# Performance work log

Measured on AMD Instinct MI355X. Metric: run time of the kernel, lower is better.

Reference implementation:

```python
import jax, jax.numpy as jnp
import numpy as np

B, C, CO = 8, 32, 32            # batch, in_channels, out_channels
NIN, NOUT, D1, D2 = 16, 10, 512, 512  # MLP dims: 16 -> 512 -> 512 -> 10 (L=3)
NRC = (NIN + 2 * NOUT + 6) * C  # rc_inp feature dim = 42*C = 1344


def _conv1(x, W, b):
    # 1x1 Conv1d: x (b, Cin, N) -> (b, Cout, N)
    return jnp.einsum('oi,bin->bon', W, x) + b[None, :, None]


def _lin(x, W, b):
    return x @ W.T + b


def setup_inputs() -> dict:
    key = jax.random.key(0)
    ks = iter(jax.random.split(key, 64))
    def rn(shape, s=1.0):
        return jax.random.normal(next(ks), shape, dtype=jnp.float32) * s
    return {
        'w0': rn((B, C, D1, NIN)), 'w1': rn((B, C, D2, D1)), 'w2': rn((B, C, NOUT, D2)),
        'b0': rn((B, C, D1)), 'b1': rn((B, C, D2)), 'b2': rn((B, C, NOUT)),
        'W_w0_rpt': rn((NIN * CO, (NIN + 2) * C), 0.02), 'B_w0_rpt': rn((NIN * CO,), 0.02),
        'W_w0_rc': rn((NIN * CO, NRC), 0.02), 'B_w0_rc': rn((NIN * CO,), 0.02),
        'W_b0': rn((CO, (NIN + 2) * C), 0.02), 'B_b0': rn((CO,), 0.02),
        'W_b0_rc': rn((CO, NRC), 0.02), 'B_b0_rc': rn((CO,), 0.02),
        'W_l1': rn((CO, C), 0.02), 'B_l1': rn((CO,), 0.02),
        'W_l1_rc': rn((CO, NRC), 0.02), 'B_l1_rc': rn((CO,), 0.02),
        'W_l1_r': rn((CO, (3 + NIN) * C), 0.02), 'B_l1_r': rn((CO,), 0.02),
        'W_l1_c': rn((CO, (3 + NOUT) * C), 0.02), 'B_l1_c': rn((CO,), 0.02),
        'W_bias1': rn((CO, (3 + NOUT) * C), 0.02), 'B_bias1': rn((CO,), 0.02),
        'W_bias1_rc': rn((CO, NRC), 0.02), 'B_bias1_rc': rn((CO,), 0.02),
        'W_fin_cpt': rn((NOUT * CO, (NOUT + 1) * C), 0.02), 'B_fin_cpt': rn((NOUT * CO,), 0.02),
        'W_fin_rc': rn((NOUT * CO, NRC), 0.02), 'B_fin_rc': rn((NOUT * CO,), 0.02),
        'W_bfin_rc': rn((NOUT * CO, NRC), 0.02), 'B_bfin_rc': rn((NOUT * CO,), 0.02),
    }


def reference(w0, w1, w2, b0, b1, b2,
              W_w0_rpt, B_w0_rpt, W_w0_rc, B_w0_rc, W_b0, B_b0, W_b0_rc, B_b0_rc,
              W_l1, B_l1, W_l1_rc, B_l1_rc, W_l1_r, B_l1_r, W_l1_c, B_l1_c,
              W_bias1, B_bias1, W_bias1_rc, B_bias1_rc,
              W_fin_cpt, B_fin_cpt, W_fin_rc, B_fin_rc, W_bfin_rc, B_bfin_rc):
    b = w0.shape[0]
    cm0, cm1, cm2 = w0.mean(-1), w1.mean(-1), w2.mean(-1)  # col means (b,c,n_row)
    rm0, rm1, rm2 = w0.mean(-2), w1.mean(-2), w2.mean(-2)  # row means (b,c,n_col)
    rc = jnp.concatenate([
        w0.mean((-1, -2)), w1.mean((-1, -2)), w2.mean((-1, -2)),
        b0.mean(-1), b1.mean(-1), b2.mean(-1),
        rm0.reshape(b, -1), cm2.reshape(b, -1), b2.reshape(b, -1)], axis=-1)  # (b, NRC)
    # ---- layer 0 (row-pointwise + rc broadcast) ----
    rpt = jnp.concatenate([jnp.swapaxes(w0, -1, -2).reshape(b, C * NIN, D1), rm1, b0], axis=1)
    z0 = _conv1(rpt, W_w0_rpt, B_w0_rpt) + _lin(rc, W_w0_rc, B_w0_rc)[..., None]
    zw0 = jnp.swapaxes(z0.reshape(b, CO, NIN, D1), -1, -2)  # (b, co, D1, NIN)
    u0 = _conv1(rpt, W_b0, B_b0) + _lin(rc, W_b0_rc, B_b0_rc)[..., None]  # (b, co, D1)
    # ---- middle layer (pointwise + rc + row + col broadcasts) ----
    row_b = jnp.concatenate([rm1, cm0, b0, jnp.swapaxes(w0, -1, -2).reshape(b, C * NIN, D1)], axis=1)
    col_b = jnp.concatenate([cm1, b1, rm2, w2.reshape(b, C * NOUT, D2)], axis=1)
    zw1 = (jnp.einsum('oi,bihw->bohw', W_l1, w1) + B_l1[None, :, None, None]
           + _lin(rc, W_l1_rc, B_l1_rc)[..., None, None]
           + _conv1(row_b, W_l1_r, B_l1_r)[:, :, None, :]
           + _conv1(col_b, W_l1_c, B_l1_c)[:, :, :, None])  # (b, co, D2, D1)
    u1 = _conv1(col_b, W_bias1, B_bias1) + _lin(rc, W_bias1_rc, B_bias1_rc)[..., None]  # (b, co, D2)
    # ---- final layer (col-pointwise + rc broadcast) ----
    cpt = jnp.concatenate([w2.reshape(b, C * NOUT, D2), cm1], axis=1)
    zf = _conv1(cpt, W_fin_cpt, B_fin_cpt) + _lin(rc, W_fin_rc, B_fin_rc)[..., None]
    zw2 = zf.reshape(b, CO, NOUT, D2)
    u2 = _lin(rc, W_bfin_rc, B_bfin_rc).reshape(b, CO, NOUT)
    return (zw0, zw1, zw2, u0, u1, u2)
```

## Files before the change

### kernel.cpp

```cpp
#include <hip/hip_runtime.h>

#define OUT_ZW1 2097152u
#define OUT_ZW2 69206016u
#define OUT_U0  70516736u
#define OUT_U1  70647808u
#define OUT_U2  70778880u

#define WS_RM1      0u
#define WS_CM1      131072u
#define WS_CM0      262144u
#define WS_RM2      393216u
#define WS_CM2      524288u
#define WS_RC       526848u
#define WS_TW0      537600u
#define WS_TB0      541696u
#define WS_TL1      541952u
#define WS_TBIAS1   542208u
#define WS_TFIN     542464u
#define WS_RTERM    545024u
#define WS_CTERM    676096u
#define WS_W0T      807168u
#define WS_WT_L1    3330304u

static __device__ __forceinline__ float wave_reduce(float v) {
#pragma unroll
  for (int off = 32; off > 0; off >>= 1) v += __shfl_down(v, off);
  return v;
}

__global__ __launch_bounds__(256) void kprep(
    const float* __restrict__ w0, const float* __restrict__ W_l1,
    float* __restrict__ ws) {
  int blk = blockIdx.x, tid = threadIdx.x;
  if (blk < 554) {
    int i = blk * 256 + tid;
    if (i < 131072) ws[WS_RM1 + i] = 0.f;
    else ws[WS_RC + (i - 131072)] = 0.f;
  } else if (blk < 558) {
    int idx = (blk - 554) * 256 + tid;
    int r = idx >> 5, c = idx & 31;
    ws[WS_WT_L1 + c * 32 + r] = W_l1[idx];
  } else {
    int bc = blk - 558;
    int b = bc >> 5, c = bc & 31;
    for (int k = 0; k < 16; ++k)
      for (int d = tid; d < 512; d += 256)
        ws[WS_W0T + ((size_t)(b * 512 + c * 16 + k)) * 512 + d] =
            w0[((size_t)bc * 512 + d) * 16 + k];
  }
}

__global__ __launch_bounds__(256) void kstats2(
    const float* __restrict__ w0, const float* __restrict__ w2,
    const float* __restrict__ b0, const float* __restrict__ b1,
    const float* __restrict__ b2, const float* __restrict__ w1,
    float* __restrict__ cm0, float* __restrict__ rm2, float* __restrict__ cm2,
    float* __restrict__ rm1, float* __restrict__ cm1, float* __restrict__ rc) {
  __shared__ float sred[16];
  __shared__ float stot;
  __shared__ float rpart[512];
  int tid = threadIdx.x, lane = tid & 63;

  if (blockIdx.x < 256) {
    int bc = blockIdx.x;
    int b = bc >> 5, c = bc & 31;
    float* rcb = rc + b * 1344;

    if (tid < 16) sred[tid] = 0.f;
    if (tid == 0) stot = 0.f;
    __syncthreads();
    {
      float rm0p[16];
#pragma unroll
      for (int k = 0; k < 16; ++k) rm0p[k] = 0.f;
      float tot = 0.f;
      for (int d = tid; d < 512; d += 256) {
        const float4* p = (const float4*)(w0 + ((size_t)bc * 512 + d) * 16);
        float s = 0.f;
#pragma unroll
        for (int q = 0; q < 4; ++q) {
          float4 v = p[q];
          s += v.x + v.y + v.z + v.w;
          rm0p[q * 4 + 0] += v.x; rm0p[q * 4 + 1] += v.y;
          rm0p[q * 4 + 2] += v.z; rm0p[q * 4 + 3] += v.w;
        }
        cm0[(size_t)bc * 512 + d] = s * (1.f / 16.f);
        tot += s;
      }
#pragma unroll
      for (int k = 0; k < 16; ++k) {
        float r = wave_reduce(rm0p[k]);
        if (lane == 0) atomicAdd(&sred[k], r);
      }
      float rt = wave_reduce(tot);
      if (lane == 0) atomicAdd(&stot, rt);
    }
    __syncthreads();
    if (tid < 16) rcb[192 + c * 16 + tid] = sred[tid] * (1.f / 512.f);
    if (tid == 0) rcb[c] = stot * (1.f / 8192.f);
    __syncthreads();

    if (tid < 10) sred[tid] = 0.f;
    if (tid == 0) stot = 0.f;
    __syncthreads();
    {
      float cm2p[10];
#pragma unroll
      for (int k = 0; k < 10; ++k) cm2p[k] = 0.f;
      float tot = 0.f;
      for (int d = tid; d < 512; d += 256) {
        float s = 0.f;
#pragma unroll
        for (int k = 0; k < 10; ++k) {
          float v = w2[((size_t)bc * 10 + k) * 512 + d];
          s += v; cm2p[k] += v;
        }
        rm2[(size_t)bc * 512 + d] = s * 0.1f;
        tot += s;
      }
#pragma unroll
      for (int k = 0; k < 10; ++k) {
        float r = wave_reduce(cm2p[k]);
        if (lane == 0) atomicAdd(&sred[k], r);
      }
      float rt = wave_reduce(tot);
      if (lane == 0) atomicAdd(&stot, rt);
    }
    __syncthreads();
    if (tid < 10) {
      float m = sred[tid] * (1.f / 512.f);
      cm2[bc * 10 + tid] = m;
      rcb[704 + c * 10 + tid] = m;
    }
    if (tid == 0) rcb[64 + c] = stot * (1.f / 5120.f);
    __syncthreads();

    if (tid < 2) sred[tid] = 0.f;
    __syncthreads();
    {
      float t0 = 0.f, t1 = 0.f;
      for (int d = tid; d < 512; d += 256) {
        t0 += b0[(size_t)bc * 512 + d];
        t1 += b1[(size_t)bc * 512 + d];
      }
      t0 = wave_reduce(t0); t1 = wave_reduce(t1);
      if (lane == 0) { atomicAdd(&sred[0], t0); atomicAdd(&sred[1], t1); }
    }
    __syncthreads();
    if (tid == 0) {
      rcb[96 + c] = sred[0] * (1.f / 512.f);
      rcb[128 + c] = sred[1] * (1.f / 512.f);
    }

    float vb2 = 0.f;
    if (tid < 10) {
      vb2 = b2[bc * 10 + tid];
      rcb[1024 + c * 10 + tid] = vb2;
    }
    if (tid < 64) {
      float s = wave_reduce(vb2);
      if (tid == 0) rcb[160 + c] = s * 0.1f;
    }
  } else {
    int idx = blockIdx.x - 256;
    int bc = idx >> 2, hc = idx & 3;
    int b = bc >> 5, c = bc & 31;
    int wid = tid >> 6;
    const float* base = w1 + (size_t)bc * 262144 + (size_t)hc * 128 * 512;
    float col0 = 0.f, col1 = 0.f;
    for (int hl = 0; hl < 128; ++hl) {
      float2 x = *(const float2*)(base + hl * 512 + 2 * tid);
      col0 += x.x; col1 += x.y;
      float r = wave_reduce(x.x + x.y);
      if (lane == 0) rpart[hl * 4 + wid] = r;
    }
    __syncthreads();
    if (tid < 128) {
      float s = rpart[tid * 4] + rpart[tid * 4 + 1] + rpart[tid * 4 + 2] + rpart[tid * 4 + 3];
      cm1[(size_t)bc * 512 + hc * 128 + tid] = s * (1.f / 512.f);
    }
    atomicAdd(&rm1[(size_t)bc * 512 + 2 * tid], col0);
    atomicAdd(&rm1[(size_t)bc * 512 + 2 * tid + 1], col1);
    float bt = wave_reduce(col0 + col1);
    if (lane == 0) atomicAdd(&rc[b * 1344 + 32 + c], bt * (1.f / 262144.f));
  }
}

__global__ __launch_bounds__(256) void krcgemm(
    const float* __restrict__ rc,
    const float* __restrict__ W_w0_rc, const float* __restrict__ B_w0_rc,
    const float* __restrict__ W_b0_rc, const float* __restrict__ B_b0_rc,
    const float* __restrict__ W_l1_rc, const float* __restrict__ B_l1_rc,
    const float* __restrict__ W_bias1_rc, const float* __restrict__ B_bias1_rc,
    const float* __restrict__ W_fin_rc, const float* __restrict__ B_fin_rc,
    const float* __restrict__ W_bfin_rc, const float* __restrict__ B_bfin_rc,
    float* __restrict__ t_w0, float* __restrict__ t_b0, float* __restrict__ t_l1,
    float* __restrict__ t_bias1, float* __restrict__ t_fin, float* __restrict__ u2out) {
  int blk = blockIdx.x;
  int b = blk / 312;
  int tid = threadIdx.x, lane = tid & 63, wid = tid >> 6;
  int r = (blk % 312) * 4 + wid;
  __shared__ float rcs[1344];
  for (int i = tid; i < 1344; i += 256) rcs[i] = rc[b * 1344 + i];
  __syncthreads();
  const float* W; const float* Bb; float* dst; int row;
  if (r < 512)      { W = W_w0_rc;    Bb = B_w0_rc;    row = r;       dst = t_w0 + b * 512; }
  else if (r < 544) { W = W_b0_rc;    Bb = B_b0_rc;    row = r - 512; dst = t_b0 + b * 32; }
  else if (r < 576) { W = W_l1_rc;    Bb = B_l1_rc;    row = r - 544; dst = t_l1 + b * 32; }
  else if (r < 608) { W = W_bias1_rc; Bb = B_bias1_rc; row = r - 576; dst = t_bias1 + b * 32; }
  else if (r < 928) { W = W_fin_rc;   Bb = B_fin_rc;   row = r - 608; dst = t_fin + b * 320; }
  else              { W = W_bfin_rc;  Bb = B_bfin_rc;  row = r - 928; dst = u2out + b * 320; }
  const float* wr = W + (size_t)row * 1344;
  float acc = 0.f;
  for (int j = lane; j < 1344; j += 64) acc += wr[j] * rcs[j];
  acc = wave_reduce(acc);
  if (lane == 0) dst[row] = acc + Bb[row];
}

__global__ __launch_bounds__(256) void kbig(
    const float* __restrict__ rm1, const float* __restrict__ cm0,
    const float* __restrict__ b0, const float* __restrict__ w0T,
    const float* __restrict__ W_l1_r, const float* __restrict__ B_l1_r,
    float* __restrict__ rterm,
    const float* __restrict__ cm1, const float* __restrict__ b1,
    const float* __restrict__ rm2, const float* __restrict__ w2,
    const float* __restrict__ W_l1_c, const float* __restrict__ B_l1_c,
    const float* __restrict__ B_l1, const float* __restrict__ t_l1,
    const float* __restrict__ W_bias1, const float* __restrict__ B_bias1,
    const float* __restrict__ t_bias1,
    float* __restrict__ cterm_full, float* __restrict__ u1out,
    const float* __restrict__ W_w0_rpt, const float* __restrict__ B_rpt,
    const float* __restrict__ W_b0, const float* __restrict__ B_b0w,
    const float* __restrict__ t_w0, const float* __restrict__ t_b0,
    const float* __restrict__ W_fin_cpt, const float* __restrict__ B_fin,
    const float* __restrict__ t_fin, float* __restrict__ out) {
  __shared__ float wlds[6656];
  int bid = blockIdx.x, tid = threadIdx.x;

  if (bid < 128) {
    int x = bid & 1, oy = (bid >> 1) & 7, b = bid >> 4;
    int p = x * 256 + tid;
    if (oy < 4) {
      int o0 = oy * 8;
      for (int idx = tid; idx < 608 * 8; idx += 256) {
        int i = idx >> 3, oo = idx & 7;
        wlds[idx] = W_l1_r[(size_t)(o0 + oo) * 608 + i];
      }
      __syncthreads();
      float acc[8] = {0, 0, 0, 0, 0, 0, 0, 0};
#pragma unroll 4
      for (int i = 0; i < 32; ++i) {
        float xv = rm1[((size_t)b * 32 + i) * 512 + p] * (1.f / 512.f);
        float4 wa = *(const float4*)&wlds[i * 8];
        float4 wb = *(const float4*)&wlds[i * 8 + 4];
        acc[0] += wa.x * xv; acc[1] += wa.y * xv; acc[2] += wa.z * xv; acc[3] += wa.w * xv;
        acc[4] += wb.x * xv; acc[5] += wb.y * xv; acc[6] += wb.z * xv; acc[7] += wb.w * xv;
      }
#pragma unroll 4
      for (int i = 0; i < 32; ++i) {
        float xv = cm0[((size_t)b * 32 + i) * 512 + p];
        float4 wa = *(const float4*)&wlds[(32 + i) * 8];
        float4 wb = *(const float4*)&wlds[(32 + i) * 8 + 4];
        acc[0] += wa.x * xv; acc[1] += wa.y * xv; acc[2] += wa.z * xv; acc[3] += wa.w * xv;
        acc[4] += wb.x * xv; acc[5] += wb.y * xv; acc[6] += wb.z * xv; acc[7] += wb.w * xv;
      }
#pragma unroll 4
      for (int i = 0; i < 32; ++i) {
        float xv = b0[((size_t)b * 32 + i) * 512 + p];
        float4 wa = *(const float4*)&wlds[(64 + i) * 8];
        float4 wb = *(const float4*)&wlds[(64 + i) * 8 + 4];
        acc[0] += wa.x * xv; acc[1] += wa.y * xv; acc[2] += wa.z * xv; acc[3] += wa.w * xv;
        acc[4] += wb.x * xv; acc[5] += wb.y * xv; acc[6] += wb.z * xv; acc[7] += wb.w * xv;
      }
      const float* xp = w0T + (size_t)b * 512 * 512 + p;
#pragma unroll 4
      for (int i = 0; i < 512; ++i) {
        float xv = xp[(size_t)i * 512];
        float4 wa = *(const float4*)&wlds[(96 + i) * 8];
        float4 wb = *(const float4*)&wlds[(96 + i) * 8 + 4];
        acc[0] += wa.x * xv; acc[1] += wa.y * xv; acc[2] += wa.z * xv; acc[3] += wa.w * xv;
        acc[4] += wb.x * xv; acc[5] += wb.y * xv; acc[6] += wb.z * xv; acc[7] += wb.w * xv;
      }
#pragma unroll
      for (int oo = 0; oo < 8; ++oo) {
        int o = o0 + oo;
        rterm[((size_t)b * 32 + o) * 512 + p] = acc[oo] + B_l1_r[o];
      }
    } else {
      int o0 = (oy - 4) * 8;
      for (int idx = tid; idx < 416 * 8; idx += 256) {
        int i = idx >> 3, oo = idx & 7;
        wlds[idx] = W_l1_c[(size_t)(o0 + oo) * 416 + i];
        wlds[3328 + idx] = W_bias1[(size_t)(o0 + oo) * 416 + i];
      }
      __syncthreads();
      float ac[8] = {0, 0, 0, 0, 0, 0, 0, 0};
      float au[8] = {0, 0, 0, 0, 0, 0, 0, 0};
#pragma unroll 4
      for (int i = 0; i < 32; ++i) {
        float xv = cm1[((size_t)b * 32 + i) * 512 + p];
        float4 wa = *(const float4*)&wlds[i * 8];
        float4 wb = *(const float4*)&wlds[i * 8 + 4];
        float4 va = *(const float4*)&wlds[3328 + i * 8];
        float4 vb = *(const float4*)&wlds[3328 + i * 8 + 4];
        ac[0] += wa.x * xv; ac[1] += wa.y * xv; ac[2] += wa.z * xv; ac[3] += wa.w * xv;
        ac[4] += wb.x * xv; ac[5] += wb.y * xv; ac[6] += wb.z * xv; ac[7] += wb.w * xv;
        au[0] += va.x * xv; au[1] += va.y * xv; au[2] += va.z * xv; au[3] += va.w * xv;
        au[4] += vb.x * xv; au[5] += vb.y * xv; au[6] += vb.z * xv; au[7] += vb.w * xv;
      }
#pragma unroll 4
      for (int i = 0; i < 32; ++i) {
        float xv = b1[((size_t)b * 32 + i) * 512 + p];
        float4 wa = *(const float4*)&wlds[(32 + i) * 8];
        float4 wb = *(const float4*)&wlds[(32 + i) * 8 + 4];
        float4 va = *(const float4*)&wlds[3328 + (32 + i) * 8];
        float4 vb = *(const float4*)&wlds[3328 + (32 + i) * 8 + 4];
        ac[0] += wa.x * xv; ac[1] += wa.y * xv; ac[2] += wa.z * xv; ac[3] += wa.w * xv;
        ac[4] += wb.x * xv; ac[5] += wb.y * xv; ac[6] += wb.z * xv; ac[7] += wb.w * xv;
        au[0] += va.x * xv; au[1] += va.y * xv; au[2] += va.z * xv; au[3] += va.w * xv;
        au[4] += vb.x * xv; au[5] += vb.y * xv; au[6] += vb.z * xv; au[7] += vb.w * xv;
      }
#pragma unroll 4
      for (int i = 0; i < 32; ++i) {
        float xv = rm2[((size_t)b * 32 + i) * 512 + p];
        float4 wa = *(const float4*)&wlds[(64 + i) * 8];
        float4 wb = *(const float4*)&wlds[(64 + i) * 8 + 4];
        float4 va = *(const float4*)&wlds[3328 + (64 + i) * 8];
        float4 vb = *(const float4*)&wlds[3328 + (64 + i) * 8 + 4];
        ac[0] += wa.x * xv; ac[1] += wa.y * xv; ac[2] += wa.z * xv; ac[3] += wa.w * xv;
        ac[4] += wb.x * xv; ac[5] += wb.y * xv; ac[6] += wb.z * xv; ac[7] += wb.w * xv;
        au[0] += va.x * xv; au[1] += va.y * xv; au[2] += va.z * xv; au[3] += va.w * xv;
        au[4] += vb.x * xv; au[5] += vb.y * xv; au[6] += vb.z * xv; au[7] += vb.w * xv;
      }
      const float* xp = w2 + (size_t)b * 320 * 512 + p;
#pragma unroll 4
      for (int i = 0; i < 320; ++i) {
        float xv = xp[(size_t)i * 512];
        float4 wa = *(const float4*)&wlds[(96 + i) * 8];
        float4 wb = *(const float4*)&wlds[(96 + i) * 8 + 4];
        float4 va = *(const float4*)&wlds[3328 + (96 + i) * 8];
        float4 vb = *(const float4*)&wlds[3328 + (96 + i) * 8 + 4];
        ac[0] += wa.x * xv; ac[1] += wa.y * xv; ac[2] += wa.z * xv; ac[3] += wa.w * xv;
        ac[4] += wb.x * xv; ac[5] += wb.y * xv; ac[6] += wb.z * xv; ac[7] += wb.w * xv;
        au[0] += va.x * xv; au[1] += va.y * xv; au[2] += va.z * xv; au[3] += va.w * xv;
        au[4] += vb.x * xv; au[5] += vb.y * xv; au[6] += vb.z * xv; au[7] += vb.w * xv;
      }
#pragma unroll
      for (int oo = 0; oo < 8; ++oo) {
        int o = o0 + oo;
        cterm_full[((size_t)b * 32 + o) * 512 + p] = ac[oo] + B_l1_c[o] + B_l1[o] + t_l1[b * 32 + o];
        u1out[((size_t)b * 32 + o) * 512 + p] = au[oo] + B_bias1[o] + t_bias1[b * 32 + o];
      }
    }
  } else if (bid < 1216) {
    int t = bid - 128;
    int x = t & 1, rest = t >> 1;
    int oc = rest % 68, b = rest / 68;
    bool isZ = oc < 64;
    int o0 = isZ ? oc * 8 : (oc - 64) * 8;
    const float* Wsrc = isZ ? W_w0_rpt : W_b0;
    for (int idx = tid; idx < 576 * 8; idx += 256) {
      int i = idx >> 3, oo = idx & 7;
      wlds[idx] = Wsrc[(size_t)(o0 + oo) * 576 + i];
    }
    __syncthreads();
    int d = x * 256 + tid;
    float acc[8] = {0, 0, 0, 0, 0, 0, 0, 0};
    const float* xp = w0T + (size_t)b * 512 * 512 + d;
#pragma unroll 4
    for (int i = 0; i < 512; ++i) {
      float xv = xp[(size_t)i * 512];
      float4 wa = *(const float4*)&wlds[i * 8];
      float4 wb = *(const float4*)&wlds[i * 8 + 4];
      acc[0] += wa.x * xv; acc[1] += wa.y * xv; acc[2] += wa.z * xv; acc[3] += wa.w * xv;
      acc[4] += wb.x * xv; acc[5] += wb.y * xv; acc[6] += wb.z * xv; acc[7] += wb.w * xv;
    }
#pragma unroll 4
    for (int i = 0; i < 32; ++i) {
      float xv = rm1[((size_t)b * 32 + i) * 512 + d] * (1.f / 512.f);
      float4 wa = *(const float4*)&wlds[(512 + i) * 8];
      float4 wb = *(const float4*)&wlds[(512 + i) * 8 + 4];
      acc[0] += wa.x * xv; acc[1] += wa.y * xv; acc[2] += wa.z * xv; acc[3] += wa.w * xv;
      acc[4] += wb.x * xv; acc[5] += wb.y * xv; acc[6] += wb.z * xv; acc[7] += wb.w * xv;
    }
#pragma unroll 4
    for (int i = 0; i < 32; ++i) {
      float xv = b0[((size_t)b * 32 + i) * 512 + d];
      float4 wa = *(const float4*)&wlds[(544 + i) * 8];
      float4 wb = *(const float4*)&wlds[(544 + i) * 8 + 4];
      acc[0] += wa.x * xv; acc[1] += wa.y * xv; acc[2] += wa.z * xv; acc[3] += wa.w * xv;
      acc[4] += wb.x * xv; acc[5] += wb.y * xv; acc[6] += wb.z * xv; acc[7] += wb.w * xv;
    }
    if (isZ) {
#pragma unroll
      for (int oo = 0; oo < 8; ++oo) {
        int o = o0 + oo, co = o >> 4, k = o & 15;
        out[(((size_t)b * 32 + co) * 512 + d) * 16 + k] = acc[oo] + B_rpt[o] + t_w0[b * 512 + o];
      }
    } else {
#pragma unroll
      for (int oo = 0; oo < 8; ++oo) {
        int o = o0 + oo;
        out[OUT_U0 + ((size_t)b * 32 + o) * 512 + d] = acc[oo] + B_b0w[o] + t_b0[b * 32 + o];
      }
    }
  } else {
    int t = bid - 1216;
    int x = t & 1, rest = t >> 1;
    int oc = rest % 40, b = rest / 40;
    int o0 = oc * 8;
    for (int idx = tid; idx < 352 * 8; idx += 256) {
      int i = idx >> 3, oo = idx & 7;
      wlds[idx] = W_fin_cpt[(size_t)(o0 + oo) * 352 + i];
    }
    __syncthreads();
    int d = x * 256 + tid;
    float acc[8] = {0, 0, 0, 0, 0, 0, 0, 0};
    const float* xp = w2 + (size_t)b * 320 * 512 + d;
#pragma unroll 4
    for (int i = 0; i < 320; ++i) {
      float xv = xp[(size_t)i * 512];
      float4 wa = *(const float4*)&wlds[i * 8];
      float4 wb = *(const float4*)&wlds[i * 8 + 4];
      acc[0] += wa.x * xv; acc[1] += wa.y * xv; acc[2] += wa.z * xv; acc[3] += wa.w * xv;
      acc[4] += wb.x * xv; acc[5] += wb.y * xv; acc[6] += wb.z * xv; acc[7] += wb.w * xv;
    }
#pragma unroll 4
    for (int i = 0; i < 32; ++i) {
      float xv = cm1[((size_t)b * 32 + i) * 512 + d];
      float4 wa = *(const float4*)&wlds[(320 + i) * 8];
      float4 wb = *(const float4*)&wlds[(320 + i) * 8 + 4];
      acc[0] += wa.x * xv; acc[1] += wa.y * xv; acc[2] += wa.z * xv; acc[3] += wa.w * xv;
      acc[4] += wb.x * xv; acc[5] += wb.y * xv; acc[6] += wb.z * xv; acc[7] += wb.w * xv;
    }
#pragma unroll
    for (int oo = 0; oo < 8; ++oo) {
      int o = o0 + oo;
      out[OUT_ZW2 + ((size_t)b * 320 + o) * 512 + d] = acc[oo] + B_fin[o] + t_fin[b * 320 + o];
    }
  }
}

__global__ __launch_bounds__(256) void kzw1(
    const float* __restrict__ w1, const float* __restrict__ Wt_l1,
    const float* __restrict__ rterm, const float* __restrict__ cterm,
    float* __restrict__ out) {
  __shared__ float wl[1024];
  int hp = blockIdx.x, b = blockIdx.y;
  int t = threadIdx.x;
  for (int i = t; i < 1024; i += 256) wl[i] = Wt_l1[i];
  __syncthreads();
  int h0 = hp * 2;
  int hoff = t >> 7;
  int w = (t & 127) * 4;
  float4 acc[32];
#pragma unroll
  for (int o = 0; o < 32; ++o) acc[o] = make_float4(0.f, 0.f, 0.f, 0.f);
  const float* src = w1 + ((size_t)b * 32 * 512 + h0) * 512 + 4 * t;
#pragma unroll 4
  for (int i = 0; i < 32; ++i) {
    float4 x = *(const float4*)(src + (size_t)i * 262144);
    const float* wp = wl + i * 32;
#pragma unroll
    for (int o = 0; o < 32; ++o) {
      acc[o].x += wp[o] * x.x;
      acc[o].y += wp[o] * x.y;
      acc[o].z += wp[o] * x.z;
      acc[o].w += wp[o] * x.w;
    }
  }
  int h = h0 + hoff;
#pragma unroll
  for (int o = 0; o < 32; ++o) {
    float cf = cterm[((size_t)b * 32 + o) * 512 + h];
    float4 rt = *(const float4*)(rterm + ((size_t)b * 32 + o) * 512 + w);
    float4 res = make_float4(acc[o].x + rt.x + cf, acc[o].y + rt.y + cf,
                             acc[o].z + rt.z + cf, acc[o].w + rt.w + cf);
    *(float4*)(out + (size_t)OUT_ZW1 + (((size_t)b * 32 + o) * 512 + h) * 512 + w) = res;
  }
}

extern "C" void kernel_launch(void* const* d_in, const int* in_sizes, int n_in,
                              void* d_out, int out_size, void* d_ws, size_t ws_size,
                              hipStream_t stream) {
  const float* w0 = (const float*)d_in[0];
  const float* w1 = (const float*)d_in[1];
  const float* w2 = (const float*)d_in[2];
  const float* b0 = (const float*)d_in[3];
  const float* b1 = (const float*)d_in[4];
  const float* b2 = (const float*)d_in[5];
  const float* W_w0_rpt = (const float*)d_in[6];
  const float* B_w0_rpt = (const float*)d_in[7];
  const float* W_w0_rc = (const float*)d_in[8];
  const float* B_w0_rc = (const float*)d_in[9];
  const float* W_b0 = (const float*)d_in[10];
  const float* B_b0 = (const float*)d_in[11];
  const float* W_b0_rc = (const float*)d_in[12];
  const float* B_b0_rc = (const float*)d_in[13];
  const float* W_l1 = (const float*)d_in[14];
  const float* B_l1 = (const float*)d_in[15];
  const float* W_l1_rc = (const float*)d_in[16];
  const float* B_l1_rc = (const float*)d_in[17];
  const float* W_l1_r = (const float*)d_in[18];
  const float* B_l1_r = (const float*)d_in[19];
  const float* W_l1_c = (const float*)d_in[20];
  const float* B_l1_c = (const float*)d_in[21];
  const float* W_bias1 = (const float*)d_in[22];
  const float* B_bias1 = (const float*)d_in[23];
  const float* W_bias1_rc = (const float*)d_in[24];
  const float* B_bias1_rc = (const float*)d_in[25];
  const float* W_fin_cpt = (const float*)d_in[26];
  const float* B_fin_cpt = (const float*)d_in[27];
  const float* W_fin_rc = (const float*)d_in[28];
  const float* B_fin_rc = (const float*)d_in[29];
  const float* W_bfin_rc = (const float*)d_in[30];
  const float* B_bfin_rc = (const float*)d_in[31];
  float* ws = (float*)d_ws;
  float* out = (float*)d_out;

  kprep<<<dim3(814), 256, 0, stream>>>(w0, W_l1, ws);

  kstats2<<<dim3(1280), 256, 0, stream>>>(w0, w2, b0, b1, b2, w1, ws + WS_CM0,
                                          ws + WS_RM2, ws + WS_CM2, ws + WS_RM1,
                                          ws + WS_CM1, ws + WS_RC);

  krcgemm<<<dim3(8 * 312), 256, 0, stream>>>(
      ws + WS_RC, W_w0_rc, B_w0_rc, W_b0_rc, B_b0_rc, W_l1_rc, B_l1_rc, W_bias1_rc,
      B_bias1_rc, W_fin_rc, B_fin_rc, W_bfin_rc, B_bfin_rc, ws + WS_TW0, ws + WS_TB0,
      ws + WS_TL1, ws + WS_TBIAS1, ws + WS_TFIN, out + OUT_U2);

  kbig<<<dim3(1856), 256, 0, stream>>>(
      ws + WS_RM1, ws + WS_CM0, b0, ws + WS_W0T, W_l1_r, B_l1_r, ws + WS_RTERM,
      ws + WS_CM1, b1, ws + WS_RM2, w2, W_l1_c, B_l1_c, B_l1, ws + WS_TL1, W_bias1,
      B_bias1, ws + WS_TBIAS1, ws + WS_CTERM, out + OUT_U1,
      W_w0_rpt, B_w0_rpt, W_b0, B_b0, ws + WS_TW0, ws + WS_TB0,
      W_fin_cpt, B_fin_cpt, ws + WS_TFIN, out);

  kzw1<<<dim3(256, 8), 256, 0, stream>>>(w1, ws + WS_WT_L1, ws + WS_RTERM, ws + WS_CTERM,
                                         out);
  (void)in_sizes; (void)n_in; (void)out_size; (void)ws_size;
}
```

Before: 364.6 us.

## Fuse prep, stats and rc-GEMM kernels to cut launches and atomics

Five launches become three. The zeroing and transpose kernel is folded into the stats kernel, w0 is transposed with vectorised reads, and the W_l1 transpose is done on load inside kzw1. Atomic accumulation of rm1 and the w1 total is replaced by per-quarter partial buffers that consumers sum, which removes the zero-init pass. The separate rc GEMV kernel is removed: each kbig block computes the rc projections it needs on the fly, and extra blocks produce u2. The cost is redundant rc dot products across blocks and four reads for every rm1 value.

New measurement: 427.2 us. 17.1% more time.

```diff
diff --git a/kernel.cpp b/kernel.cpp
--- a/kernel.cpp
+++ b/kernel.cpp
@@ -6,21 +6,15 @@
 #define OUT_U1  70647808u
 #define OUT_U2  70778880u
 
-#define WS_RM1      0u
-#define WS_CM1      131072u
-#define WS_CM0      262144u
-#define WS_RM2      393216u
-#define WS_CM2      524288u
-#define WS_RC       526848u
-#define WS_TW0      537600u
-#define WS_TB0      541696u
-#define WS_TL1      541952u
-#define WS_TBIAS1   542208u
-#define WS_TFIN     542464u
-#define WS_RTERM    545024u
-#define WS_CTERM    676096u
-#define WS_W0T      807168u
-#define WS_WT_L1    3330304u
+#define WS_RM1P  0u
+#define WS_CM1   524288u
+#define WS_CM0   655360u
+#define WS_RM2   786432u
+#define WS_RCW1  917504u
+#define WS_RC    918528u
+#define WS_RTERM 929280u
+#define WS_CTERM 1060352u
+#define WS_W0T   1191424u
 
 static __device__ __forceinline__ float wave_reduce(float v) {
 #pragma unroll
@@ -28,43 +22,24 @@
   return v;
 }
 
-__global__ __launch_bounds__(256) void kprep(
-    const float* __restrict__ w0, const float* __restrict__ W_l1,
-    float* __restrict__ ws) {
-  int blk = blockIdx.x, tid = threadIdx.x;
-  if (blk < 554) {
-    int i = blk * 256 + tid;
-    if (i < 131072) ws[WS_RM1 + i] = 0.f;
-    else ws[WS_RC + (i - 131072)] = 0.f;
-  } else if (blk < 558) {
-    int idx = (blk - 554) * 256 + tid;
-    int r = idx >> 5, c = idx & 31;
-    ws[WS_WT_L1 + c * 32 + r] = W_l1[idx];
-  } else {
-    int bc = blk - 558;
-    int b = bc >> 5, c = bc & 31;
-    for (int k = 0; k < 16; ++k)
-      for (int d = tid; d < 512; d += 256)
-        ws[WS_W0T + ((size_t)(b * 512 + c * 16 + k)) * 512 + d] =
-            w0[((size_t)bc * 512 + d) * 16 + k];
-  }
-}
-
-__global__ __launch_bounds__(256) void kstats2(
+__global__ __launch_bounds__(256) void ksetup(
     const float* __restrict__ w0, const float* __restrict__ w2,
     const float* __restrict__ b0, const float* __restrict__ b1,
     const float* __restrict__ b2, const float* __restrict__ w1,
-    float* __restrict__ cm0, float* __restrict__ rm2, float* __restrict__ cm2,
-    float* __restrict__ rm1, float* __restrict__ cm1, float* __restrict__ rc) {
+    float* __restrict__ ws) {
   __shared__ float sred[16];
   __shared__ float stot;
   __shared__ float rpart[512];
+  __shared__ float swsum[4];
   int tid = threadIdx.x, lane = tid & 63;
-
-  if (blockIdx.x < 256) {
-    int bc = blockIdx.x;
+  int bx = blockIdx.x;
+
+  if (bx < 256) {
+    int bc = bx;
     int b = bc >> 5, c = bc & 31;
-    float* rcb = rc + b * 1344;
+    float* rcb = ws + WS_RC + b * 1344;
+    float* cm0 = ws + WS_CM0;
+    float* rm2 = ws + WS_RM2;
 
     if (tid < 16) sred[tid] = 0.f;
     if (tid == 0) stot = 0.f;
@@ -127,11 +102,7 @@
       if (lane == 0) atomicAdd(&stot, rt);
     }
     __syncthreads();
-    if (tid < 10) {
-      float m = sred[tid] * (1.f / 512.f);
-      cm2[bc * 10 + tid] = m;
-      rcb[704 + c * 10 + tid] = m;
-    }
+    if (tid < 10) rcb[704 + c * 10 + tid] = sred[tid] * (1.f / 512.f);
     if (tid == 0) rcb[64 + c] = stot * (1.f / 5120.f);
     __syncthreads();
 
@@ -161,12 +132,11 @@
       float s = wave_reduce(vb2);
       if (tid == 0) rcb[160 + c] = s * 0.1f;
     }
-  } else {
-    int idx = blockIdx.x - 256;
+  } else if (bx < 1280) {
+    int idx = bx - 256;
     int bc = idx >> 2, hc = idx & 3;
-    int b = bc >> 5, c = bc & 31;
     int wid = tid >> 6;
-    const float* base = w1 + (size_t)bc * 262144 + (size_t)hc * 128 * 512;
+    const float* base = w1 + (size_t)bc * 262144 + (size_t)hc * 65536;
     float col0 = 0.f, col1 = 0.f;
     for (int hl = 0; hl < 128; ++hl) {
       float2 x = *(const float2*)(base + hl * 512 + 2 * tid);
@@ -177,65 +147,72 @@
     __syncthreads();
     if (tid < 128) {
       float s = rpart[tid * 4] + rpart[tid * 4 + 1] + rpart[tid * 4 + 2] + rpart[tid * 4 + 3];
-      cm1[(size_t)bc * 512 + hc * 128 + tid] = s * (1.f / 512.f);
-    }
-    atomicAdd(&rm1[(size_t)bc * 512 + 2 * tid], col0);
-    atomicAdd(&rm1[(size_t)bc * 512 + 2 * tid + 1], col1);
+      ws[WS_CM1 + (size_t)bc * 512 + hc * 128 + tid] = s * (1.f / 512.f);
+    }
+    ws[WS_RM1P + (size_t)hc * 131072 + (size_t)bc * 512 + 2 * tid] = col0;
+    ws[WS_RM1P + (size_t)hc * 131072 + (size_t)bc * 512 + 2 * tid + 1] = col1;
     float bt = wave_reduce(col0 + col1);
-    if (lane == 0) atomicAdd(&rc[b * 1344 + 32 + c], bt * (1.f / 262144.f));
+    if (lane == 0) swsum[wid] = bt;
+    __syncthreads();
+    if (tid == 0)
+      ws[WS_RCW1 + hc * 256 + bc] = swsum[0] + swsum[1] + swsum[2] + swsum[3];
+  } else {
+    int bc = bx - 1280;
+    int b = bc >> 5, c = bc & 31;
+    for (int dd = 0; dd < 2; ++dd) {
+      int d = tid + dd * 256;
+      const float4* src = (const float4*)(w0 + ((size_t)bc * 512 + d) * 16);
+      float4 v0 = src[0], v1 = src[1], v2 = src[2], v3 = src[3];
+      float vals[16] = {v0.x, v0.y, v0.z, v0.w, v1.x, v1.y, v1.z, v1.w,
+                        v2.x, v2.y, v2.z, v2.w, v3.x, v3.y, v3.z, v3.w};
+#pragma unroll
+      for (int k = 0; k < 16; ++k)
+        ws[WS_W0T + ((size_t)(b * 512 + c * 16 + k)) * 512 + d] = vals[k];
+    }
   }
 }
 
-__global__ __launch_bounds__(256) void krcgemm(
-    const float* __restrict__ rc,
+__global__ __launch_bounds__(256) void kbig(
+    float* __restrict__ ws, float* __restrict__ out,
+    const float* __restrict__ b0, const float* __restrict__ b1,
+    const float* __restrict__ w2,
+    const float* __restrict__ W_l1_r, const float* __restrict__ B_l1_r,
+    const float* __restrict__ W_l1_c, const float* __restrict__ B_l1_c,
+    const float* __restrict__ B_l1,
+    const float* __restrict__ W_bias1, const float* __restrict__ B_bias1,
+    const float* __restrict__ W_l1_rc, const float* __restrict__ B_l1_rc,
+    const float* __restrict__ W_bias1_rc, const float* __restrict__ B_bias1_rc,
+    const float* __restrict__ W_w0_rpt, const float* __restrict__ B_w0_rpt,
+    const float* __restrict__ W_b0, const float* __restrict__ B_b0,
     const float* __restrict__ W_w0_rc, const float* __restrict__ B_w0_rc,
     const float* __restrict__ W_b0_rc, const float* __restrict__ B_b0_rc,
-    const float* __restrict__ W_l1_rc, const float* __restrict__ B_l1_rc,
-    const float* __restrict__ W_bias1_rc, const float* __restrict__ B_bias1_rc,
+    const float* __restrict__ W_fin_cpt, const float* __restrict__ B_fin_cpt,
     const float* __restrict__ W_fin_rc, const float* __restrict__ B_fin_rc,
-    const float* __restrict__ W_bfin_rc, const float* __restrict__ B_bfin_rc,
-    float* __restrict__ t_w0, float* __restrict__ t_b0, float* __restrict__ t_l1,
-    float* __restrict__ t_bias1, float* __restrict__ t_fin, float* __restrict__ u2out) {
-  int blk = blockIdx.x;
-  int b = blk / 312;
-  int tid = threadIdx.x, lane = tid & 63, wid = tid >> 6;
-  int r = (blk % 312) * 4 + wid;
+    const float* __restrict__ W_bfin_rc, const float* __restrict__ B_bfin_rc) {
+  __shared__ float wlds[6656];
   __shared__ float rcs[1344];
-  for (int i = tid; i < 1344; i += 256) rcs[i] = rc[b * 1344 + i];
-  __syncthreads();
-  const float* W; const float* Bb; float* dst; int row;
-  if (r < 512)      { W = W_w0_rc;    Bb = B_w0_rc;    row = r;       dst = t_w0 + b * 512; }
-  else if (r < 544) { W = W_b0_rc;    Bb = B_b0_rc;    row = r - 512; dst = t_b0 + b * 32; }
-  else if (r < 576) { W = W_l1_rc;    Bb = B_l1_rc;    row = r - 544; dst = t_l1 + b * 32; }
-  else if (r < 608) { W = W_bias1_rc; Bb = B_bias1_rc; row = r - 576; dst = t_bias1 + b * 32; }
-  else if (r < 928) { W = W_fin_rc;   Bb = B_fin_rc;   row = r - 608; dst = t_fin + b * 320; }
-  else              { W = W_bfin_rc;  Bb = B_bfin_rc;  row = r - 928; dst = u2out + b * 320; }
-  const float* wr = W + (size_t)row * 1344;
-  float acc = 0.f;
-  for (int j = lane; j < 1344; j += 64) acc += wr[j] * rcs[j];
-  acc = wave_reduce(acc);
-  if (lane == 0) dst[row] = acc + Bb[row];
-}
-
-__global__ __launch_bounds__(256) void kbig(
-    const float* __restrict__ rm1, const float* __restrict__ cm0,
-    const float* __restrict__ b0, const float* __restrict__ w0T,
-    const float* __restrict__ W_l1_r, const float* __restrict__ B_l1_r,
-    float* __restrict__ rterm,
-    const float* __restrict__ cm1, const float* __restrict__ b1,
-    const float* __restrict__ rm2, const float* __restrict__ w2,
-    const float* __restrict__ W_l1_c, const float* __restrict__ B_l1_c,
-    const float* __restrict__ B_l1, const float* __restrict__ t_l1,
-    const float* __restrict__ W_bias1, const float* __restrict__ B_bias1,
-    const float* __restrict__ t_bias1,
-    float* __restrict__ cterm_full, float* __restrict__ u1out,
-    const float* __restrict__ W_w0_rpt, const float* __restrict__ B_rpt,
-    const float* __restrict__ W_b0, const float* __restrict__ B_b0w,
-    const float* __restrict__ t_w0, const float* __restrict__ t_b0,
-    const float* __restrict__ W_fin_cpt, const float* __restrict__ B_fin,
-    const float* __restrict__ t_fin, float* __restrict__ out) {
-  __shared__ float wlds[6656];
+  __shared__ float tv[16];
   int bid = blockIdx.x, tid = threadIdx.x;
+  const float* p0 = ws + WS_RM1P;
+  const float* p1 = ws + WS_RM1P + 131072;
+  const float* p2 = ws + WS_RM1P + 262144;
+  const float* p3 = ws + WS_RM1P + 393216;
+  const float* cm0 = ws + WS_CM0;
+  const float* cm1 = ws + WS_CM1;
+  const float* rm2 = ws + WS_RM2;
+  const float* w0T = ws + WS_W0T;
+
+#define STAGE_RC(b_)                                                              \
+  do {                                                                            \
+    for (int j = tid; j < 1344; j += 256)                                         \
+      if (j < 32 || j >= 64) rcs[j] = ws[WS_RC + (b_) * 1344 + j];                \
+    if (tid < 32)                                                                 \
+      rcs[32 + tid] = (ws[WS_RCW1 + 0 * 256 + (b_) * 32 + tid] +                  \
+                       ws[WS_RCW1 + 1 * 256 + (b_) * 32 + tid] +                  \
+                       ws[WS_RCW1 + 2 * 256 + (b_) * 32 + tid] +                  \
+                       ws[WS_RCW1 + 3 * 256 + (b_) * 32 + tid]) *                 \
+                      (1.f / 262144.f);                                           \
+  } while (0)
 
   if (bid < 128) {
     int x = bid & 1, oy = (bid >> 1) & 7, b = bid >> 4;
@@ -250,7 +227,8 @@
       float acc[8] = {0, 0, 0, 0, 0, 0, 0, 0};
 #pragma unroll 4
       for (int i = 0; i < 32; ++i) {
-        float xv = rm1[((size_t)b * 32 + i) * 512 + p] * (1.f / 512.f);
+        size_t off = ((size_t)b * 32 + i) * 512 + p;
+        float xv = (p0[off] + p1[off] + p2[off] + p3[off]) * (1.f / 512.f);
         float4 wa = *(const float4*)&wlds[i * 8];
         float4 wb = *(const float4*)&wlds[i * 8 + 4];
         acc[0] += wa.x * xv; acc[1] += wa.y * xv; acc[2] += wa.z * xv; acc[3] += wa.w * xv;
@@ -284,7 +262,7 @@
 #pragma unroll
       for (int oo = 0; oo < 8; ++oo) {
         int o = o0 + oo;
-        rterm[((size_t)b * 32 + o) * 512 + p] = acc[oo] + B_l1_r[o];
+        ws[WS_RTERM + ((size_t)b * 32 + o) * 512 + p] = acc[oo] + B_l1_r[o];
       }
     } else {
       int o0 = (oy - 4) * 8;
@@ -292,6 +270,19 @@
         int i = idx >> 3, oo = idx & 7;
         wlds[idx] = W_l1_c[(size_t)(o0 + oo) * 416 + i];
         wlds[3328 + idx] = W_bias1[(size_t)(o0 + oo) * 416 + i];
+      }
+      STAGE_RC(b);
+      __syncthreads();
+      {
+        int g = tid >> 4, l = tid & 15;
+        const float* wr = (g < 8) ? (W_l1_rc + (size_t)(o0 + g) * 1344)
+                                  : (W_bias1_rc + (size_t)(o0 + g - 8) * 1344);
+        float a = 0.f;
+        for (int j = l; j < 1344; j += 16) a += wr[j] * rcs[j];
+        a += __shfl_xor(a, 8); a += __shfl_xor(a, 4);
+        a += __shfl_xor(a, 2); a += __shfl_xor(a, 1);
+        if (l == 0)
+          tv[g] = a + ((g < 8) ? B_l1_rc[o0 + g] : B_bias1_rc[o0 + g - 8]);
       }
       __syncthreads();
       float ac[8] = {0, 0, 0, 0, 0, 0, 0, 0};
@@ -348,8 +339,8 @@
 #pragma unroll
       for (int oo = 0; oo < 8; ++oo) {
         int o = o0 + oo;
-        cterm_full[((size_t)b * 32 + o) * 512 + p] = ac[oo] + B_l1_c[o] + B_l1[o] + t_l1[b * 32 + o];
-        u1out[((size_t)b * 32 + o) * 512 + p] = au[oo] + B_bias1[o] + t_bias1[b * 32 + o];
+        ws[WS_CTERM + ((size_t)b * 32 + o) * 512 + p] = ac[oo] + B_l1_c[o] + B_l1[o] + tv[oo];
+        out[OUT_U1 + ((size_t)b * 32 + o) * 512 + p] = au[oo] + B_bias1[o] + tv[8 + oo];
       }
     }
   } else if (bid < 1216) {
@@ -359,9 +350,22 @@
     bool isZ = oc < 64;
     int o0 = isZ ? oc * 8 : (oc - 64) * 8;
     const float* Wsrc = isZ ? W_w0_rpt : W_b0;
+    const float* Wrc = isZ ? W_w0_rc : W_b0_rc;
+    const float* Brc = isZ ? B_w0_rc : B_b0_rc;
     for (int idx = tid; idx < 576 * 8; idx += 256) {
       int i = idx >> 3, oo = idx & 7;
       wlds[idx] = Wsrc[(size_t)(o0 + oo) * 576 + i];
+    }
+    STAGE_RC(b);
+    __syncthreads();
+    {
+      int g = tid >> 5, l = tid & 31;
+      const float* wr = Wrc + (size_t)(o0 + g) * 1344;
+      float a = 0.f;
+      for (int j = l; j < 1344; j += 32) a += wr[j] * rcs[j];
+      a += __shfl_xor(a, 16); a += __shfl_xor(a, 8); a += __shfl_xor(a, 4);
+      a += __shfl_xor(a, 2); a += __shfl_xor(a, 1);
+      if (l == 0) tv[g] = a + Brc[o0 + g];
     }
     __syncthreads();
     int d = x * 256 + tid;
@@ -377,7 +381,8 @@
     }
 #pragma unroll 4
     for (int i = 0; i < 32; ++i) {
-      float xv = rm1[((size_t)b * 32 + i) * 512 + d] * (1.f / 512.f);
+      size_t off = ((size_t)b * 32 + i) * 512 + d;
+      float xv = (p0[off] + p1[off] + p2[off] + p3[off]) * (1.f / 512.f);
       float4 wa = *(const float4*)&wlds[(512 + i) * 8];
       float4 wb = *(const float4*)&wlds[(512 + i) * 8 + 4];
       acc[0] += wa.x * xv; acc[1] += wa.y * xv; acc[2] += wa.z * xv; acc[3] += wa.w * xv;
@@ -395,16 +400,16 @@
 #pragma unroll
       for (int oo = 0; oo < 8; ++oo) {
         int o = o0 + oo, co = o >> 4, k = o & 15;
-        out[(((size_t)b * 32 + co) * 512 + d) * 16 + k] = acc[oo] + B_rpt[o] + t_w0[b * 512 + o];
+        out[(((size_t)b * 32 + co) * 512 + d) * 16 + k] = acc[oo] + B_w0_rpt[o] + tv[oo];
       }
     } else {
 #pragma unroll
       for (int oo = 0; oo < 8; ++oo) {
         int o = o0 + oo;
-        out[OUT_U0 + ((size_t)b * 32 + o) * 512 + d] = acc[oo] + B_b0w[o] + t_b0[b * 32 + o];
-      }
-    }
-  } else {
+        out[OUT_U0 + ((size_t)b * 32 + o) * 512 + d] = acc[oo] + B_b0[o] + tv[oo];
+      }
+    }
+  } else if (bid < 1856) {
     int t = bid - 1216;
     int x = t & 1, rest = t >> 1;
     int oc = rest % 40, b = rest / 40;
@@ -413,6 +418,17 @@
       int i = idx >> 3, oo = idx & 7;
       wlds[idx] = W_fin_cpt[(size_t)(o0 + oo) * 352 + i];
     }
+    STAGE_RC(b);
+    __syncthreads();
+    {
+      int g = tid >> 5, l = tid & 31;
+      const float* wr = W_fin_rc + (size_t)(o0 + g) * 1344;
+      float a = 0.f;
+      for (int j = l; j < 1344; j += 32) a += wr[j] * rcs[j];
+      a += __shfl_xor(a, 16); a += __shfl_xor(a, 8); a += __shfl_xor(a, 4);
+      a += __shfl_xor(a, 2); a += __shfl_xor(a, 1);
+      if (l == 0) tv[g] = a + B_fin_rc[o0 + g];
+    }
     __syncthreads();
     int d = x * 256 + tid;
     float acc[8] = {0, 0, 0, 0, 0, 0, 0, 0};
@@ -436,19 +452,30 @@
 #pragma unroll
     for (int oo = 0; oo < 8; ++oo) {
       int o = o0 + oo;
-      out[OUT_ZW2 + ((size_t)b * 320 + o) * 512 + d] = acc[oo] + B_fin[o] + t_fin[b * 320 + o];
+      out[OUT_ZW2 + ((size_t)b * 320 + o) * 512 + d] = acc[oo] + B_fin_cpt[o] + tv[oo];
+    }
+  } else {
+    int b = bid - 1856;
+    STAGE_RC(b);
+    __syncthreads();
+    for (int r = tid; r < 320; r += 256) {
+      const float* wr = W_bfin_rc + (size_t)r * 1344;
+      float a = 0.f;
+      for (int j = 0; j < 1344; ++j) a += wr[j] * rcs[j];
+      out[OUT_U2 + (size_t)b * 320 + r] = a + B_bfin_rc[r];
     }
   }
+#undef STAGE_RC
 }
 
 __global__ __launch_bounds__(256) void kzw1(
-    const float* __restrict__ w1, const float* __restrict__ Wt_l1,
+    const float* __restrict__ w1, const float* __restrict__ W_l1,
     const float* __restrict__ rterm, const float* __restrict__ cterm,
     float* __restrict__ out) {
   __shared__ float wl[1024];
   int hp = blockIdx.x, b = blockIdx.y;
   int t = threadIdx.x;
-  for (int i = t; i < 1024; i += 256) wl[i] = Wt_l1[i];
+  for (int i = t; i < 1024; i += 256) wl[(i & 31) * 32 + (i >> 5)] = W_l1[i];
   __syncthreads();
   int h0 = hp * 2;
   int hoff = t >> 7;
@@ -518,25 +545,14 @@
   float* ws = (float*)d_ws;
   float* out = (float*)d_out;
 
-  kprep<<<dim3(814), 256, 0, stream>>>(w0, W_l1, ws);
-
-  kstats2<<<dim3(1280), 256, 0, stream>>>(w0, w2, b0, b1, b2, w1, ws + WS_CM0,
-                                          ws + WS_RM2, ws + WS_CM2, ws + WS_RM1,
-                                          ws + WS_CM1, ws + WS_RC);
-
-  krcgemm<<<dim3(8 * 312), 256, 0, stream>>>(
-      ws + WS_RC, W_w0_rc, B_w0_rc, W_b0_rc, B_b0_rc, W_l1_rc, B_l1_rc, W_bias1_rc,
-      B_bias1_rc, W_fin_rc, B_fin_rc, W_bfin_rc, B_bfin_rc, ws + WS_TW0, ws + WS_TB0,
-      ws + WS_TL1, ws + WS_TBIAS1, ws + WS_TFIN, out + OUT_U2);
-
-  kbig<<<dim3(1856), 256, 0, stream>>>(
-      ws + WS_RM1, ws + WS_CM0, b0, ws + WS_W0T, W_l1_r, B_l1_r, ws + WS_RTERM,
-      ws + WS_CM1, b1, ws + WS_RM2, w2, W_l1_c, B_l1_c, B_l1, ws + WS_TL1, W_bias1,
-      B_bias1, ws + WS_TBIAS1, ws + WS_CTERM, out + OUT_U1,
-      W_w0_rpt, B_w0_rpt, W_b0, B_b0, ws + WS_TW0, ws + WS_TB0,
-      W_fin_cpt, B_fin_cpt, ws + WS_TFIN, out);
-
-  kzw1<<<dim3(256, 8), 256, 0, stream>>>(w1, ws + WS_WT_L1, ws + WS_RTERM, ws + WS_CTERM,
-                                         out);
+  ksetup<<<dim3(1536), 256, 0, stream>>>(w0, w2, b0, b1, b2, w1, ws);
+
+  kbig<<<dim3(1864), 256, 0, stream>>>(
+      ws, out, b0, b1, w2, W_l1_r, B_l1_r, W_l1_c, B_l1_c, B_l1, W_bias1, B_bias1,
+      W_l1_rc, B_l1_rc, W_bias1_rc, B_bias1_rc, W_w0_rpt, B_w0_rpt, W_b0, B_b0,
+      W_w0_rc, B_w0_rc, W_b0_rc, B_b0_rc, W_fin_cpt, B_fin_cpt, W_fin_rc, B_fin_rc,
+      W_bfin_rc, B_bfin_rc);
+
+  kzw1<<<dim3(256, 8), 256, 0, stream>>>(w1, W_l1, ws + WS_RTERM, ws + WS_CTERM, out);
   (void)in_sizes; (void)n_in; (void)out_size; (void)ws_size;
 }
```

## Merge prep into stats kernel and replace atomics with partial-sum buffers

Applied to the files above, without the earlier changes.

Removes the separate prep kernel. The w0 transpose moves into the stats kernel as extra blocks and now uses vectorized float4 reads, and the W_l1 transpose is done at LDS-load time inside kzw1. The rm1 and rc atomics are replaced by per-chunk partial buffers, which are reduced later in added krcgemm blocks and its rc staging. This cuts one launch, the zeroing pass and global atomic contention, at the cost of extra workspace traffic for the partials.

After: 360.7 us. No clear change (-1.1%).

```diff
diff --git a/kernel.cpp b/kernel.cpp
--- a/kernel.cpp
+++ b/kernel.cpp
@@ -6,21 +6,20 @@
 #define OUT_U1  70647808u
 #define OUT_U2  70778880u
 
-#define WS_RM1      0u
-#define WS_CM1      131072u
-#define WS_CM0      262144u
-#define WS_RM2      393216u
-#define WS_CM2      524288u
-#define WS_RC       526848u
-#define WS_TW0      537600u
-#define WS_TB0      541696u
-#define WS_TL1      541952u
-#define WS_TBIAS1   542208u
-#define WS_TFIN     542464u
-#define WS_RTERM    545024u
-#define WS_CTERM    676096u
-#define WS_W0T      807168u
-#define WS_WT_L1    3330304u
+#define WS_RM1P   0u
+#define WS_CM1    524288u
+#define WS_CM0    655360u
+#define WS_RM2    786432u
+#define WS_RCW1   917504u
+#define WS_RC     918528u
+#define WS_RTERM  929280u
+#define WS_CTERM  1060352u
+#define WS_W0T    1191424u
+#define WS_TW0    3288576u
+#define WS_TB0    3292672u
+#define WS_TL1    3292928u
+#define WS_TBIAS1 3293184u
+#define WS_TFIN   3293440u
 
 static __device__ __forceinline__ float wave_reduce(float v) {
 #pragma unroll
@@ -28,43 +27,24 @@
   return v;
 }
 
-__global__ __launch_bounds__(256) void kprep(
-    const float* __restrict__ w0, const float* __restrict__ W_l1,
-    float* __restrict__ ws) {
-  int blk = blockIdx.x, tid = threadIdx.x;
-  if (blk < 554) {
-    int i = blk * 256 + tid;
-    if (i < 131072) ws[WS_RM1 + i] = 0.f;
-    else ws[WS_RC + (i - 131072)] = 0.f;
-  } else if (blk < 558) {
-    int idx = (blk - 554) * 256 + tid;
-    int r = idx >> 5, c = idx & 31;
-    ws[WS_WT_L1 + c * 32 + r] = W_l1[idx];
-  } else {
-    int bc = blk - 558;
-    int b = bc >> 5, c = bc & 31;
-    for (int k = 0; k < 16; ++k)
-      for (int d = tid; d < 512; d += 256)
-        ws[WS_W0T + ((size_t)(b * 512 + c * 16 + k)) * 512 + d] =
-            w0[((size_t)bc * 512 + d) * 16 + k];
-  }
-}
-
-__global__ __launch_bounds__(256) void kstats2(
+__global__ __launch_bounds__(256) void ksetup(
     const float* __restrict__ w0, const float* __restrict__ w2,
     const float* __restrict__ b0, const float* __restrict__ b1,
     const float* __restrict__ b2, const float* __restrict__ w1,
-    float* __restrict__ cm0, float* __restrict__ rm2, float* __restrict__ cm2,
-    float* __restrict__ rm1, float* __restrict__ cm1, float* __restrict__ rc) {
+    float* __restrict__ ws) {
   __shared__ float sred[16];
   __shared__ float stot;
   __shared__ float rpart[512];
+  __shared__ float swsum[4];
   int tid = threadIdx.x, lane = tid & 63;
-
-  if (blockIdx.x < 256) {
-    int bc = blockIdx.x;
+  int bx = blockIdx.x;
+
+  if (bx < 256) {
+    int bc = bx;
     int b = bc >> 5, c = bc & 31;
-    float* rcb = rc + b * 1344;
+    float* rcb = ws + WS_RC + b * 1344;
+    float* cm0 = ws + WS_CM0;
+    float* rm2 = ws + WS_RM2;
 
     if (tid < 16) sred[tid] = 0.f;
     if (tid == 0) stot = 0.f;
@@ -127,11 +107,7 @@
       if (lane == 0) atomicAdd(&stot, rt);
     }
     __syncthreads();
-    if (tid < 10) {
-      float m = sred[tid] * (1.f / 512.f);
-      cm2[bc * 10 + tid] = m;
-      rcb[704 + c * 10 + tid] = m;
-    }
+    if (tid < 10) rcb[704 + c * 10 + tid] = sred[tid] * (1.f / 512.f);
     if (tid == 0) rcb[64 + c] = stot * (1.f / 5120.f);
     __syncthreads();
 
@@ -161,12 +137,11 @@
       float s = wave_reduce(vb2);
       if (tid == 0) rcb[160 + c] = s * 0.1f;
     }
-  } else {
-    int idx = blockIdx.x - 256;
+  } else if (bx < 1280) {
+    int idx = bx - 256;
     int bc = idx >> 2, hc = idx & 3;
-    int b = bc >> 5, c = bc & 31;
     int wid = tid >> 6;
-    const float* base = w1 + (size_t)bc * 262144 + (size_t)hc * 128 * 512;
+    const float* base = w1 + (size_t)bc * 262144 + (size_t)hc * 65536;
     float col0 = 0.f, col1 = 0.f;
     for (int hl = 0; hl < 128; ++hl) {
       float2 x = *(const float2*)(base + hl * 512 + 2 * tid);
@@ -177,38 +152,65 @@
     __syncthreads();
     if (tid < 128) {
       float s = rpart[tid * 4] + rpart[tid * 4 + 1] + rpart[tid * 4 + 2] + rpart[tid * 4 + 3];
-      cm1[(size_t)bc * 512 + hc * 128 + tid] = s * (1.f / 512.f);
-    }
-    atomicAdd(&rm1[(size_t)bc * 512 + 2 * tid], col0);
-    atomicAdd(&rm1[(size_t)bc * 512 + 2 * tid + 1], col1);
+      ws[WS_CM1 + (size_t)bc * 512 + hc * 128 + tid] = s * (1.f / 512.f);
+    }
+    ws[WS_RM1P + (size_t)hc * 131072 + (size_t)bc * 512 + 2 * tid] = col0;
+    ws[WS_RM1P + (size_t)hc * 131072 + (size_t)bc * 512 + 2 * tid + 1] = col1;
     float bt = wave_reduce(col0 + col1);
-    if (lane == 0) atomicAdd(&rc[b * 1344 + 32 + c], bt * (1.f / 262144.f));
+    if (lane == 0) swsum[wid] = bt;
+    __syncthreads();
+    if (tid == 0)
+      ws[WS_RCW1 + hc * 256 + bc] = swsum[0] + swsum[1] + swsum[2] + swsum[3];
+  } else {
+    int bc = bx - 1280;
+    int b = bc >> 5, c = bc & 31;
+    for (int dd = 0; dd < 2; ++dd) {
+      int d = tid + dd * 256;
+      const float4* src = (const float4*)(w0 + ((size_t)bc * 512 + d) * 16);
+      float4 v0 = src[0], v1 = src[1], v2 = src[2], v3 = src[3];
+      float vals[16] = {v0.x, v0.y, v0.z, v0.w, v1.x, v1.y, v1.z, v1.w,
+                        v2.x, v2.y, v2.z, v2.w, v3.x, v3.y, v3.z, v3.w};
+#pragma unroll
+      for (int k = 0; k < 16; ++k)
+        ws[WS_W0T + ((size_t)(b * 512 + c * 16 + k)) * 512 + d] = vals[k];
+    }
   }
 }
 
 __global__ __launch_bounds__(256) void krcgemm(
-    const float* __restrict__ rc,
+    float* __restrict__ ws,
     const float* __restrict__ W_w0_rc, const float* __restrict__ B_w0_rc,
     const float* __restrict__ W_b0_rc, const float* __restrict__ B_b0_rc,
     const float* __restrict__ W_l1_rc, const float* __restrict__ B_l1_rc,
     const float* __restrict__ W_bias1_rc, const float* __restrict__ B_bias1_rc,
     const float* __restrict__ W_fin_rc, const float* __restrict__ B_fin_rc,
     const float* __restrict__ W_bfin_rc, const float* __restrict__ B_bfin_rc,
-    float* __restrict__ t_w0, float* __restrict__ t_b0, float* __restrict__ t_l1,
-    float* __restrict__ t_bias1, float* __restrict__ t_fin, float* __restrict__ u2out) {
-  int blk = blockIdx.x;
+    float* __restrict__ u2out) {
+  int blk = blockIdx.x, tid = threadIdx.x;
+  if (blk >= 2496) {
+    int i = (blk - 2496) * 256 + tid;
+    ws[WS_RM1P + i] = ws[WS_RM1P + i] + ws[WS_RM1P + 131072 + i] +
+                      ws[WS_RM1P + 262144 + i] + ws[WS_RM1P + 393216 + i];
+    return;
+  }
   int b = blk / 312;
-  int tid = threadIdx.x, lane = tid & 63, wid = tid >> 6;
+  int lane = tid & 63, wid = tid >> 6;
   int r = (blk % 312) * 4 + wid;
   __shared__ float rcs[1344];
-  for (int i = tid; i < 1344; i += 256) rcs[i] = rc[b * 1344 + i];
+  for (int j = tid; j < 1344; j += 256)
+    if (j < 32 || j >= 64) rcs[j] = ws[WS_RC + b * 1344 + j];
+  if (tid < 32)
+    rcs[32 + tid] = (ws[WS_RCW1 + 0 * 256 + b * 32 + tid] +
+                     ws[WS_RCW1 + 1 * 256 + b * 32 + tid] +
+                     ws[WS_RCW1 + 2 * 256 + b * 32 + tid] +
+                     ws[WS_RCW1 + 3 * 256 + b * 32 + tid]) * (1.f / 262144.f);
   __syncthreads();
   const float* W; const float* Bb; float* dst; int row;
-  if (r < 512)      { W = W_w0_rc;    Bb = B_w0_rc;    row = r;       dst = t_w0 + b * 512; }
-  else if (r < 544) { W = W_b0_rc;    Bb = B_b0_rc;    row = r - 512; dst = t_b0 + b * 32; }
-  else if (r < 576) { W = W_l1_rc;    Bb = B_l1_rc;    row = r - 544; dst = t_l1 + b * 32; }
-  else if (r < 608) { W = W_bias1_rc; Bb = B_bias1_rc; row = r - 576; dst = t_bias1 + b * 32; }
-  else if (r < 928) { W = W_fin_rc;   Bb = B_fin_rc;   row = r - 608; dst = t_fin + b * 320; }
+  if (r < 512)      { W = W_w0_rc;    Bb = B_w0_rc;    row = r;       dst = ws + WS_TW0 + b * 512; }
+  else if (r < 544) { W = W_b0_rc;    Bb = B_b0_rc;    row = r - 512; dst = ws + WS_TB0 + b * 32; }
+  else if (r < 576) { W = W_l1_rc;    Bb = B_l1_rc;    row = r - 544; dst = ws + WS_TL1 + b * 32; }
+  else if (r < 608) { W = W_bias1_rc; Bb = B_bias1_rc; row = r - 576; dst = ws + WS_TBIAS1 + b * 32; }
+  else if (r < 928) { W = W_fin_rc;   Bb = B_fin_rc;   row = r - 608; dst = ws + WS_TFIN + b * 320; }
   else              { W = W_bfin_rc;  Bb = B_bfin_rc;  row = r - 928; dst = u2out + b * 320; }
   const float* wr = W + (size_t)row * 1344;
   float acc = 0.f;
@@ -442,13 +444,13 @@
 }
 
 __global__ __launch_bounds__(256) void kzw1(
-    const float* __restrict__ w1, const float* __restrict__ Wt_l1,
+    const float* __restrict__ w1, const float* __restrict__ W_l1,
     const float* __restrict__ rterm, const float* __restrict__ cterm,
     float* __restrict__ out) {
   __shared__ float wl[1024];
   int hp = blockIdx.x, b = blockIdx.y;
   int t = threadIdx.x;
-  for (int i = t; i < 1024; i += 256) wl[i] = Wt_l1[i];
+  for (int i = t; i < 1024; i += 256) wl[(i & 31) * 32 + (i >> 5)] = W_l1[i];
   __syncthreads();
   int h0 = hp * 2;
   int hoff = t >> 7;
@@ -518,25 +520,19 @@
   float* ws = (float*)d_ws;
   float* out = (float*)d_out;
 
-  kprep<<<dim3(814), 256, 0, stream>>>(w0, W_l1, ws);
-
-  kstats2<<<dim3(1280), 256, 0, stream>>>(w0, w2, b0, b1, b2, w1, ws + WS_CM0,
-                                          ws + WS_RM2, ws + WS_CM2, ws + WS_RM1,
-                                          ws + WS_CM1, ws + WS_RC);
-
-  krcgemm<<<dim3(8 * 312), 256, 0, stream>>>(
-      ws + WS_RC, W_w0_rc, B_w0_rc, W_b0_rc, B_b0_rc, W_l1_rc, B_l1_rc, W_bias1_rc,
-      B_bias1_rc, W_fin_rc, B_fin_rc, W_bfin_rc, B_bfin_rc, ws + WS_TW0, ws + WS_TB0,
-      ws + WS_TL1, ws + WS_TBIAS1, ws + WS_TFIN, out + OUT_U2);
+  ksetup<<<dim3(1536), 256, 0, stream>>>(w0, w2, b0, b1, b2, w1, ws);
+
+  krcgemm<<<dim3(3008), 256, 0, stream>>>(
+      ws, W_w0_rc, B_w0_rc, W_b0_rc, B_b0_rc, W_l1_rc, B_l1_rc, W_bias1_rc,
+      B_bias1_rc, W_fin_rc, B_fin_rc, W_bfin_rc, B_bfin_rc, out + OUT_U2);
 
   kbig<<<dim3(1856), 256, 0, stream>>>(
-      ws + WS_RM1, ws + WS_CM0, b0, ws + WS_W0T, W_l1_r, B_l1_r, ws + WS_RTERM,
+      ws + WS_RM1P, ws + WS_CM0, b0, ws + WS_W0T, W_l1_r, B_l1_r, ws + WS_RTERM,
       ws + WS_CM1, b1, ws + WS_RM2, w2, W_l1_c, B_l1_c, B_l1, ws + WS_TL1, W_bias1,
       B_bias1, ws + WS_TBIAS1, ws + WS_CTERM, out + OUT_U1,
       W_w0_rpt, B_w0_rpt, W_b0, B_b0, ws + WS_TW0, ws + WS_TB0,
       W_fin_cpt, B_fin_cpt, ws + WS_TFIN, out);
 
-  kzw1<<<dim3(256, 8), 256, 0, stream>>>(w1, ws + WS_WT_L1, ws + WS_RTERM, ws + WS_CTERM,
-                                         out);
+  kzw1<<<dim3(256, 8), 256, 0, stream>>>(w1, W_l1, ws + WS_RTERM, ws + WS_CTERM, out);
   (void)in_sizes; (void)n_in; (void)out_size; (void)ws_size;
 }
```
